# Kernel tuning notes

Hardware: AMD Instinct MI355X
Metric: run time of the kernel (lower is better)

## Reference

```python
import jax, jax.numpy as jnp
import numpy as np

N = 262144   # nodes
E = 4194304  # edges (avg degree 16)
G = 1024     # graphs in batch
F_IN, F_GCN, F_DENSE = 3, 16, 16
NEG_SLOPE = 0.01  # nn.LeakyReLU default


def _leaky(x):
    return jax.nn.leaky_relu(x, NEG_SLOPE)


def _gcn_conv(x, W, b, src, dst, ew):
    """PyG GCNConv: h = x @ W; symmetric deg-norm with self-loops (weight 1);
    out[i] = sum_{(j->i)} norm_e * h[j] + (1/deg_i) * h[i] + b."""
    h = x @ W                                   # [N, out]
    deg = jax.ops.segment_sum(ew, dst, num_segments=N) + 1.0  # +1 from self-loop
    dinv = jnp.where(deg > 0, jax.lax.rsqrt(deg), 0.0)        # deg^{-1/2}
    norm = dinv[src] * ew * dinv[dst]           # [E]
    agg = jax.ops.segment_sum(h[src] * norm[:, None], dst, num_segments=N)
    agg = agg + h * (dinv * dinv)[:, None]      # self-loop message, norm = 1/deg
    return agg + b


def setup_inputs() -> dict:
    key = jax.random.key(0)
    ks = jax.random.split(key, 24)
    inp = {
        "X": jax.random.normal(ks[0], (N, F_IN), dtype=jnp.float32),
        "Edge_index": jax.random.randint(ks[1], (2, E), 0, N, dtype=jnp.int64) if jax.config.jax_enable_x64 else jax.random.randint(ks[1], (2, E), 0, N, dtype=jnp.int32),
        "Edge_weight": jax.random.uniform(ks[2], (E,), dtype=jnp.float32),
        "Batching": jnp.sort(jax.random.randint(ks[3], (N,), 0, G, dtype=jnp.int32)),
        "num_graphs": G,
    }
    def lin(k, fi, fo):
        kw, kb = jax.random.split(k)
        s = 1.0 / np.sqrt(fi)
        return (jax.random.uniform(kw, (fi, fo), minval=-s, maxval=s, dtype=jnp.float32),
                jax.random.uniform(kb, (fo,), minval=-s, maxval=s, dtype=jnp.float32))
    inp["W1"], inp["b1"] = lin(ks[4], F_IN, F_GCN)
    inp["W2"], inp["b2"] = lin(ks[5], F_GCN, F_GCN)
    inp["Wp1"], inp["bp1"] = lin(ks[6], F_GCN, F_DENSE)
    inp["Wp2"], inp["bp2"] = lin(ks[7], F_DENSE, F_DENSE)
    inp["Wp3"], inp["bp3"] = lin(ks[8], F_DENSE, 2)
    inp["Wt1"], inp["bt1"] = lin(ks[9], F_GCN, F_DENSE)
    inp["Wt2"], inp["bt2"] = lin(ks[10], F_DENSE, F_DENSE)
    inp["Wt3"], inp["bt3"] = lin(ks[11], F_DENSE, 2)
    return inp


def reference(X, Edge_index, Edge_weight, Batching, num_graphs,
              W1, b1, W2, b2,
              Wp1, bp1, Wp2, bp2, Wp3, bp3,
              Wt1, bt1, Wt2, bt2, Wt3, bt3):
    src, dst = Edge_index[0], Edge_index[1]
    out = _leaky(_gcn_conv(X, W1, b1, src, dst, Edge_weight))
    out = _leaky(_gcn_conv(out, W2, b2, src, dst, Edge_weight))
    # global mean pool over graphs
    sums = jax.ops.segment_sum(out, Batching, num_segments=num_graphs)
    cnt = jax.ops.segment_sum(jnp.ones((out.shape[0],), out.dtype), Batching,
                              num_segments=num_graphs)
    pooled = sums / jnp.maximum(cnt, 1.0)[:, None]   # [G, 16]
    Phi = _leaky(pooled @ Wp1 + bp1)
    Phi = _leaky(Phi @ Wp2 + bp2)
    Phi = Phi @ Wp3 + bp3
    Theta = _leaky(pooled @ Wt1 + bt1)
    Theta = _leaky(Theta @ Wt2 + bt2)
    Theta = Theta @ Wt3 + bt3
    return jnp.concatenate((Phi, Theta), axis=1)   # [G, 4]
```

## Files before the change

### kernel.cpp

```cpp
#include <hip/hip_runtime.h>


#define NBUCK 512
#define BCAP  10240
#define CHUNK 4096
#define NTILE 8
#define TSH   15
#define RCAP  20

__device__ __forceinline__ float leaky(float x) { return x > 0.f ? x : 0.01f * x; }

__global__ __launch_bounds__(256) void
binA_kernel(const int* __restrict__ src, const int* __restrict__ dst,
            const float* __restrict__ ew, int* __restrict__ bucketCursor,
            int2* __restrict__ coarse, int E) {
    __shared__ int lhist[NBUCK], lbase[NBUCK], lcur[NBUCK], gbase[NBUCK];
    __shared__ int tmp[256];
    __shared__ int2 stag[CHUNK];
    __shared__ unsigned short sbuck[CHUNK];
    int t = threadIdx.x;
    int base = blockIdx.x * CHUNK;
    for (int b = t; b < NBUCK; b += 256) { lhist[b] = 0; lcur[b] = 0; }
    __syncthreads();
    int n = min(CHUNK, E - base);
    int myDst[16], mySrc[16]; float myEw[16];
#pragma unroll
    for (int k = 0; k < 16; ++k) {
        int j = t + k * 256;
        if (j < n) {
            int d = dst[base + j];
            myDst[k] = d; mySrc[k] = src[base + j]; myEw[k] = ew[base + j];
            atomicAdd(&lhist[d >> 9], 1);
        } else myDst[k] = -1;
    }
    __syncthreads();
    tmp[t] = lhist[2 * t] + lhist[2 * t + 1];
    __syncthreads();
    for (int off = 1; off < 256; off <<= 1) {
        int v = (t >= off) ? tmp[t - off] : 0;
        __syncthreads();
        tmp[t] += v;
        __syncthreads();
    }
    int pb = (t == 0) ? 0 : tmp[t - 1];
    lbase[2 * t] = pb;
    lbase[2 * t + 1] = pb + lhist[2 * t];
    __syncthreads();
    for (int b = t; b < NBUCK; b += 256) {
        int c = lhist[b];
        gbase[b] = c ? atomicAdd(&bucketCursor[b], c) : 0;
    }
    for (int k = 0; k < 16; ++k) {
        int d = myDst[k];
        if (d >= 0) {
            int b = d >> 9;
            int p = lbase[b] + atomicAdd(&lcur[b], 1);
            stag[p] = make_int2(mySrc[k] | ((d & 511) << 18), __float_as_int(myEw[k]));
            sbuck[p] = (unsigned short)b;
        }
    }
    __syncthreads();
    for (int j = t; j < n; j += 256) {
        int b = sbuck[j];
        coarse[(size_t)b * BCAP + gbase[b] + (j - lbase[b])] = stag[j];
    }
}

__global__ void bscan_kernel(const int* __restrict__ bucketCursor,
                             int* __restrict__ bucketBase, int* __restrict__ row,
                             int N, int E) {
    __shared__ int s[NBUCK];
    int t = threadIdx.x;
    int v = bucketCursor[t];
    s[t] = v;
    __syncthreads();
    for (int off = 1; off < NBUCK; off <<= 1) {
        int x = (t >= off) ? s[t - off] : 0;
        __syncthreads();
        s[t] += x;
        __syncthreads();
    }
    bucketBase[t] = s[t] - v;
    if (t == 0) row[N] = E;
}

__global__ __launch_bounds__(512, 2) void
binB_kernel(const int* __restrict__ bucketCursor, const int* __restrict__ bucketBase,
            const int2* __restrict__ coarse, int2* __restrict__ edata,
            int* __restrict__ row, float* __restrict__ dinv,
            uint4* __restrict__ tcnt) {
    __shared__ int2 sedata[BCAP];
    __shared__ int loff[NBUCK * NTILE];
    __shared__ int tmp[512];
    int b = blockIdx.x, t = threadIdx.x;
    for (int i = t; i < NBUCK * NTILE; i += 512) loff[i] = 0;
    __syncthreads();
    int cnt = bucketCursor[b];
    int gb  = bucketBase[b];
    const int2* cb = coarse + (size_t)b * BCAP;
    int2 myE[RCAP]; int myKey[RCAP];
#pragma unroll
    for (int k = 0; k < RCAP; ++k) {
        int j = t + k * 512;
        if (j < cnt) {
            int2 e = cb[j];
            myE[k] = e;
            myKey[k] = (((e.x >> 18) & 511) << 3) | ((e.x & 0x3FFFF) >> TSH);
            atomicAdd(&loff[myKey[k]], 1);
        } else myKey[k] = -1;
    }
    __syncthreads();
    int base8 = t * 8, s = 0;
#pragma unroll
    for (int k = 0; k < 8; ++k) s += loff[base8 + k];
    tmp[t] = s;
    __syncthreads();
    for (int off = 1; off < 512; off <<= 1) {
        int v = (t >= off) ? tmp[t - off] : 0;
        __syncthreads();
        tmp[t] += v;
        __syncthreads();
    }
    int run = tmp[t] - s;
    int o[9];
#pragma unroll
    for (int k = 0; k < 8; ++k) { int v = loff[base8 + k]; o[k] = run; loff[base8 + k] = run; run += v; }
    o[8] = run;
    __syncthreads();
    int node = b * 512 + t;
    row[node] = gb + o[0];
    uint4 p;
    p.x = (unsigned)(o[1] - o[0]) | ((unsigned)(o[2] - o[1]) << 16);
    p.y = (unsigned)(o[3] - o[2]) | ((unsigned)(o[4] - o[3]) << 16);
    p.z = (unsigned)(o[5] - o[4]) | ((unsigned)(o[6] - o[5]) << 16);
    p.w = (unsigned)(o[7] - o[6]) | ((unsigned)(o[8] - o[7]) << 16);
    tcnt[node] = p;
#pragma unroll
    for (int k = 0; k < RCAP; ++k) {
        if (myKey[k] >= 0) {
            int pos = atomicAdd(&loff[myKey[k]], 1);
            sedata[pos] = make_int2(myE[k].x & 0x3FFFF, myE[k].y);
        }
    }
    __syncthreads();
    for (int j = t; j < cnt; j += 512) edata[gb + j] = sedata[j];
    float dsum = 0.f;
    for (int j = o[0]; j < o[8]; ++j) dsum += __int_as_float(sedata[j].y);
    dinv[node] = rsqrtf(1.0f + dsum);
}

__global__ void node1_kernel(const float* __restrict__ X, const float* __restrict__ W1,
                             const float* __restrict__ dinv, float* __restrict__ h, int N) {
    __shared__ float w[48];
    if (threadIdx.x < 48) w[threadIdx.x] = W1[threadIdx.x];
    __syncthreads();
    int i = blockIdx.x * blockDim.x + threadIdx.x;
    if (i >= N) return;
    float x0 = X[3 * i], x1 = X[3 * i + 1], x2 = X[3 * i + 2];
    float di = dinv[i];
    float4* hp = (float4*)(h + (size_t)i * 16);
#pragma unroll
    for (int k = 0; k < 4; ++k) {
        float4 v;
        v.x = (x0 * w[4 * k + 0] + x1 * w[16 + 4 * k + 0] + x2 * w[32 + 4 * k + 0]) * di;
        v.y = (x0 * w[4 * k + 1] + x1 * w[16 + 4 * k + 1] + x2 * w[32 + 4 * k + 1]) * di;
        v.z = (x0 * w[4 * k + 2] + x1 * w[16 + 4 * k + 2] + x2 * w[32 + 4 * k + 2]) * di;
        v.w = (x0 * w[4 * k + 3] + x1 * w[16 + 4 * k + 3] + x2 * w[32 + 4 * k + 3]) * di;
        hp[k] = v;
    }
}

__global__ __launch_bounds__(512) void
aggA_kernel(const int* __restrict__ row, const uint4* __restrict__ tcnt,
            const int2* __restrict__ edata, const float* __restrict__ dinv,
            const float* __restrict__ hprime, const float* __restrict__ b1,
            const float* __restrict__ W2, float* __restrict__ h2) {
    __shared__ float w[256];
    __shared__ float bb[16];
    __shared__ float sx[128][17];
    int t = threadIdx.x;
    if (t < 256) w[t] = W2[t];
    else if (t < 272) bb[t - 256] = b1[t - 256];
    int ln = t >> 2, l = t & 3;
    int iA = blockIdx.x * 256 + ln, iB = iA + 128;
    const float4* hp = (const float4*)hprime;
    int eA = row[iA], eB = row[iB];
    uint4 cAv = tcnt[iA], cBv = tcnt[iB];
    unsigned ca[4] = {cAv.x, cAv.y, cAv.z, cAv.w};
    unsigned cb[4] = {cBv.x, cBv.y, cBv.z, cBv.w};
    float diA = dinv[iA], diB = dinv[iB];
    float4 accA = hp[(size_t)iA * 4 + l];
    float4 accB = hp[(size_t)iB * 4 + l];
#pragma unroll
    for (int tt = 0; tt < NTILE; ++tt) {
        int nA = (ca[tt >> 1] >> ((tt & 1) * 16)) & 0xFFFF;
        int nB = (cb[tt >> 1] >> ((tt & 1) * 16)) & 0xFFFF;
        for (int e = eA + nA; eA < e; ++eA) {
            int2 ed = edata[eA];
            float ewv = __int_as_float(ed.y);
            float4 v = hp[(size_t)ed.x * 4 + l];
            accA.x += v.x * ewv; accA.y += v.y * ewv;
            accA.z += v.z * ewv; accA.w += v.w * ewv;
        }
        for (int e = eB + nB; eB < e; ++eB) {
            int2 ed = edata[eB];
            float ewv = __int_as_float(ed.y);
            float4 v = hp[(size_t)ed.x * 4 + l];
            accB.x += v.x * ewv; accB.y += v.y * ewv;
            accB.z += v.z * ewv; accB.w += v.w * ewv;
        }
        __syncthreads();
    }
    sx[ln][4 * l + 0] = leaky(diA * accA.x + bb[4 * l + 0]);
    sx[ln][4 * l + 1] = leaky(diA * accA.y + bb[4 * l + 1]);
    sx[ln][4 * l + 2] = leaky(diA * accA.z + bb[4 * l + 2]);
    sx[ln][4 * l + 3] = leaky(diA * accA.w + bb[4 * l + 3]);
    __syncthreads();
    {
        float a0 = 0.f, a1 = 0.f, a2 = 0.f, a3 = 0.f;
#pragma unroll
        for (int q = 0; q < 16; ++q) {
            float xv = sx[ln][q];
            a0 += xv * w[q * 16 + 4 * l + 0];
            a1 += xv * w[q * 16 + 4 * l + 1];
            a2 += xv * w[q * 16 + 4 * l + 2];
            a3 += xv * w[q * 16 + 4 * l + 3];
        }
        ((float4*)h2)[(size_t)iA * 4 + l] = make_float4(a0 * diA, a1 * diA, a2 * diA, a3 * diA);
    }
    __syncthreads();
    sx[ln][4 * l + 0] = leaky(diB * accB.x + bb[4 * l + 0]);
    sx[ln][4 * l + 1] = leaky(diB * accB.y + bb[4 * l + 1]);
    sx[ln][4 * l + 2] = leaky(diB * accB.z + bb[4 * l + 2]);
    sx[ln][4 * l + 3] = leaky(diB * accB.w + bb[4 * l + 3]);
    __syncthreads();
    {
        float a0 = 0.f, a1 = 0.f, a2 = 0.f, a3 = 0.f;
#pragma unroll
        for (int q = 0; q < 16; ++q) {
            float xv = sx[ln][q];
            a0 += xv * w[q * 16 + 4 * l + 0];
            a1 += xv * w[q * 16 + 4 * l + 1];
            a2 += xv * w[q * 16 + 4 * l + 2];
            a3 += xv * w[q * 16 + 4 * l + 3];
        }
        ((float4*)h2)[(size_t)iB * 4 + l] = make_float4(a0 * diB, a1 * diB, a2 * diB, a3 * diB);
    }
}

__global__ __launch_bounds__(512) void
aggB_kernel(const int* __restrict__ row, const uint4* __restrict__ tcnt,
            const int2* __restrict__ edata, const float* __restrict__ dinv,
            const float* __restrict__ h2prime, float* __restrict__ agg2) {
    int t = threadIdx.x;
    int ln = t >> 2, l = t & 3;
    int iA = blockIdx.x * 256 + ln, iB = iA + 128;
    const float4* hp = (const float4*)h2prime;
    int eA = row[iA], eB = row[iB];
    uint4 cAv = tcnt[iA], cBv = tcnt[iB];
    unsigned ca[4] = {cAv.x, cAv.y, cAv.z, cAv.w};
    unsigned cb[4] = {cBv.x, cBv.y, cBv.z, cBv.w};
    float diA = dinv[iA], diB = dinv[iB];
    float4 accA = hp[(size_t)iA * 4 + l];
    float4 accB = hp[(size_t)iB * 4 + l];
#pragma unroll
    for (int tt = 0; tt < NTILE; ++tt) {
        int nA = (ca[tt >> 1] >> ((tt & 1) * 16)) & 0xFFFF;
        int nB = (cb[tt >> 1] >> ((tt & 1) * 16)) & 0xFFFF;
        for (int e = eA + nA; eA < e; ++eA) {
            int2 ed = edata[eA];
            float ewv = __int_as_float(ed.y);
            float4 v = hp[(size_t)ed.x * 4 + l];
            accA.x += v.x * ewv; accA.y += v.y * ewv;
            accA.z += v.z * ewv; accA.w += v.w * ewv;
        }
        for (int e = eB + nB; eB < e; ++eB) {
            int2 ed = edata[eB];
            float ewv = __int_as_float(ed.y);
            float4 v = hp[(size_t)ed.x * 4 + l];
            accB.x += v.x * ewv; accB.y += v.y * ewv;
            accB.z += v.z * ewv; accB.w += v.w * ewv;
        }
        __syncthreads();
    }
    ((float4*)agg2)[(size_t)iA * 4 + l] =
        make_float4(accA.x * diA, accA.y * diA, accA.z * diA, accA.w * diA);
    ((float4*)agg2)[(size_t)iB * 4 + l] =
        make_float4(accB.x * diB, accB.y * diB, accB.z * diB, accB.w * diB);
}

__device__ void head_mlp(const float* pooled,
                         const float* __restrict__ Wa, const float* __restrict__ ba,
                         const float* __restrict__ Wb, const float* __restrict__ bb,
                         const float* __restrict__ Wc, const float* __restrict__ bc,
                         float* o) {
    float t[16], u[16];
#pragma unroll
    for (int f = 0; f < 16; ++f) {
        float a = ba[f];
        for (int k = 0; k < 16; ++k) a += pooled[k] * Wa[k * 16 + f];
        t[f] = leaky(a);
    }
#pragma unroll
    for (int f = 0; f < 16; ++f) {
        float a = bb[f];
        for (int k = 0; k < 16; ++k) a += t[k] * Wb[k * 16 + f];
        u[f] = leaky(a);
    }
    float o0 = bc[0], o1 = bc[1];
    for (int k = 0; k < 16; ++k) { o0 += u[k] * Wc[2 * k]; o1 += u[k] * Wc[2 * k + 1]; }
    o[0] = o0; o[1] = o1;
}

__global__ void pool_head_kernel(const float* __restrict__ agg2, const float* __restrict__ b2,
                                 const int* __restrict__ batching, int N,
                                 const float* __restrict__ Wp1, const float* __restrict__ bp1,
                                 const float* __restrict__ Wp2, const float* __restrict__ bp2,
                                 const float* __restrict__ Wp3, const float* __restrict__ bp3,
                                 const float* __restrict__ Wt1, const float* __restrict__ bt1,
                                 const float* __restrict__ Wt2, const float* __restrict__ bt2,
                                 const float* __restrict__ Wt3, const float* __restrict__ bt3,
                                 float* __restrict__ out) {
    int g = blockIdx.x;
    __shared__ int bounds[2];
    if (threadIdx.x < 2) {
        int v = g + (int)threadIdx.x;
        int lo = 0, hi = N;
        while (lo < hi) { int m = (lo + hi) >> 1; if (batching[m] < v) lo = m + 1; else hi = m; }
        bounds[threadIdx.x] = lo;
    }
    __syncthreads();
    int lo = bounds[0], hi = bounds[1];
    int f = threadIdx.x & 15, r = threadIdx.x >> 4;
    float bf = b2[f];
    float acc = 0.f;
    for (int i = lo + r; i < hi; i += 16) acc += leaky(agg2[(size_t)i * 16 + f] + bf);
    __shared__ float red[16][17];
    red[r][f] = acc;
    __syncthreads();
    __shared__ float pooled[16];
    if (r == 0) {
        float s = 0.f;
#pragma unroll
        for (int k = 0; k < 16; ++k) s += red[k][f];
        pooled[f] = s / fmaxf((float)(hi - lo), 1.0f);
    }
    __syncthreads();
    if (threadIdx.x == 0) {
        float o[2];
        head_mlp(pooled, Wp1, bp1, Wp2, bp2, Wp3, bp3, o);
        out[4 * g + 0] = o[0]; out[4 * g + 1] = o[1];
    } else if (threadIdx.x == 1) {
        float o[2];
        head_mlp(pooled, Wt1, bt1, Wt2, bt2, Wt3, bt3, o);
        out[4 * g + 2] = o[0]; out[4 * g + 3] = o[1];
    }
}

extern "C" void kernel_launch(void* const* d_in, const int* in_sizes, int n_in,
                              void* d_out, int out_size, void* d_ws, size_t ws_size,
                              hipStream_t stream) {
    const float* X        = (const float*)d_in[0];
    const int*   ei       = (const int*)d_in[1];
    const float* ew       = (const float*)d_in[2];
    const int*   batching = (const int*)d_in[3];
    const float* W1  = (const float*)d_in[5];  const float* b1  = (const float*)d_in[6];
    const float* W2  = (const float*)d_in[7];  const float* b2  = (const float*)d_in[8];
    const float* Wp1 = (const float*)d_in[9];  const float* bp1 = (const float*)d_in[10];
    const float* Wp2 = (const float*)d_in[11]; const float* bp2 = (const float*)d_in[12];
    const float* Wp3 = (const float*)d_in[13]; const float* bp3 = (const float*)d_in[14];
    const float* Wt1 = (const float*)d_in[15]; const float* bt1 = (const float*)d_in[16];
    const float* Wt2 = (const float*)d_in[17]; const float* bt2 = (const float*)d_in[18];
    const float* Wt3 = (const float*)d_in[19]; const float* bt3 = (const float*)d_in[20];

    const int N = in_sizes[3];
    const int E = in_sizes[2];
    const int G = out_size / 4;
    const int* src = ei;
    const int* dst = ei + E;

    char* ws = (char*)d_ws;
    size_t off = 0;
    int2*  edata = (int2*)(ws + off);  off += (size_t)E * 8;
    char*  regionA = ws + off;         off += (size_t)N * 64 * 3;
    int2*  coarse = (int2*)regionA;
    float* hprime = (float*)regionA;
    float* h2     = (float*)(regionA + (size_t)N * 64);
    float* agg2   = (float*)(regionA + (size_t)N * 128);
    int*   bucketCursor = (int*)(ws + off); off += NBUCK * 4;
    int*   bucketBase   = (int*)(ws + off); off += NBUCK * 4;
    int*   row   = (int*)(ws + off);   off += (size_t)(N + 4) * 4;
    float* dinv  = (float*)(ws + off); off += (size_t)N * 4;
    uint4* tcnt  = (uint4*)(ws + off); off += (size_t)N * 16;
    float* out   = (float*)d_out;

    hipMemsetAsync(bucketCursor, 0, NBUCK * 4, stream);

    const int tb = 256;
    binA_kernel<<<(E + CHUNK - 1) / CHUNK, tb, 0, stream>>>(src, dst, ew, bucketCursor, coarse, E);
    bscan_kernel<<<1, NBUCK, 0, stream>>>(bucketCursor, bucketBase, row, N, E);
    binB_kernel<<<NBUCK, 512, 0, stream>>>(bucketCursor, bucketBase, coarse, edata, row, dinv, tcnt);
    node1_kernel<<<(N + tb - 1) / tb, tb, 0, stream>>>(X, W1, dinv, hprime, N);
    aggA_kernel<<<N / 256, 512, 0, stream>>>(row, tcnt, edata, dinv, hprime, b1, W2, h2);
    aggB_kernel<<<N / 256, 512, 0, stream>>>(row, tcnt, edata, dinv, h2, agg2);
    pool_head_kernel<<<G, tb, 0, stream>>>(agg2, b2, batching, N,
                                           Wp1, bp1, Wp2, bp2, Wp3, bp3,
                                           Wt1, bt1, Wt2, bt2, Wt3, bt3, out);
}
```

Before: 374.9 us.

## Aggregate raw 3-feature inputs in layer 1 and apply W1 on the fly

Instead of precomputing h' = X·W1·dinv as 16 floats per node, a pack kernel stores (x0,x1,x2,dinv) as one float4 per node. The first aggregation gathers that 16-byte record per edge and applies W1 in registers. This cuts gather bytes per edge and removes the 64-byte-per-node h' buffer. The tiled loop with its per-tile __syncthreads is replaced by a plain interleaved while loop over the row range. The trade-off is more FMAs per edge, and each of the 4 lanes per node redundantly gathers the same float4.

```diff
diff --git a/kernel.cpp b/kernel.cpp
--- a/kernel.cpp
+++ b/kernel.cpp
@@ -149,72 +149,70 @@
     dinv[node] = rsqrtf(1.0f + dsum);
 }
 
-__global__ void node1_kernel(const float* __restrict__ X, const float* __restrict__ W1,
-                             const float* __restrict__ dinv, float* __restrict__ h, int N) {
-    __shared__ float w[48];
-    if (threadIdx.x < 48) w[threadIdx.x] = W1[threadIdx.x];
-    __syncthreads();
+__global__ void pack_kernel(const float* __restrict__ X, const float* __restrict__ dinv,
+                            float4* __restrict__ Xp, int N) {
     int i = blockIdx.x * blockDim.x + threadIdx.x;
     if (i >= N) return;
-    float x0 = X[3 * i], x1 = X[3 * i + 1], x2 = X[3 * i + 2];
-    float di = dinv[i];
-    float4* hp = (float4*)(h + (size_t)i * 16);
-#pragma unroll
-    for (int k = 0; k < 4; ++k) {
-        float4 v;
-        v.x = (x0 * w[4 * k + 0] + x1 * w[16 + 4 * k + 0] + x2 * w[32 + 4 * k + 0]) * di;
-        v.y = (x0 * w[4 * k + 1] + x1 * w[16 + 4 * k + 1] + x2 * w[32 + 4 * k + 1]) * di;
-        v.z = (x0 * w[4 * k + 2] + x1 * w[16 + 4 * k + 2] + x2 * w[32 + 4 * k + 2]) * di;
-        v.w = (x0 * w[4 * k + 3] + x1 * w[16 + 4 * k + 3] + x2 * w[32 + 4 * k + 3]) * di;
-        hp[k] = v;
-    }
+    Xp[i] = make_float4(X[3 * i], X[3 * i + 1], X[3 * i + 2], dinv[i]);
 }
 
 __global__ __launch_bounds__(512) void
-aggA_kernel(const int* __restrict__ row, const uint4* __restrict__ tcnt,
-            const int2* __restrict__ edata, const float* __restrict__ dinv,
-            const float* __restrict__ hprime, const float* __restrict__ b1,
-            const float* __restrict__ W2, float* __restrict__ h2) {
+aggA_kernel(const int* __restrict__ row, const int2* __restrict__ edata,
+            const float4* __restrict__ Xp, const float* __restrict__ W1,
+            const float* __restrict__ b1, const float* __restrict__ W2,
+            float* __restrict__ h2) {
+    __shared__ float w1s[48];
     __shared__ float w[256];
     __shared__ float bb[16];
     __shared__ float sx[128][17];
     int t = threadIdx.x;
     if (t < 256) w[t] = W2[t];
     else if (t < 272) bb[t - 256] = b1[t - 256];
+    else if (t >= 288 && t < 336) w1s[t - 288] = W1[t - 288];
+    __syncthreads();
     int ln = t >> 2, l = t & 3;
+    float w1r0[4], w1r1[4], w1r2[4];
+#pragma unroll
+    for (int c = 0; c < 4; ++c) {
+        w1r0[c] = w1s[0 * 16 + 4 * l + c];
+        w1r1[c] = w1s[1 * 16 + 4 * l + c];
+        w1r2[c] = w1s[2 * 16 + 4 * l + c];
+    }
     int iA = blockIdx.x * 256 + ln, iB = iA + 128;
-    const float4* hp = (const float4*)hprime;
-    int eA = row[iA], eB = row[iB];
-    uint4 cAv = tcnt[iA], cBv = tcnt[iB];
-    unsigned ca[4] = {cAv.x, cAv.y, cAv.z, cAv.w};
-    unsigned cb[4] = {cBv.x, cBv.y, cBv.z, cBv.w};
-    float diA = dinv[iA], diB = dinv[iB];
-    float4 accA = hp[(size_t)iA * 4 + l];
-    float4 accB = hp[(size_t)iB * 4 + l];
-#pragma unroll
-    for (int tt = 0; tt < NTILE; ++tt) {
-        int nA = (ca[tt >> 1] >> ((tt & 1) * 16)) & 0xFFFF;
-        int nB = (cb[tt >> 1] >> ((tt & 1) * 16)) & 0xFFFF;
-        for (int e = eA + nA; eA < e; ++eA) {
-            int2 ed = edata[eA];
-            float ewv = __int_as_float(ed.y);
-            float4 v = hp[(size_t)ed.x * 4 + l];
-            accA.x += v.x * ewv; accA.y += v.y * ewv;
-            accA.z += v.z * ewv; accA.w += v.w * ewv;
-        }
-        for (int e = eB + nB; eB < e; ++eB) {
-            int2 ed = edata[eB];
-            float ewv = __int_as_float(ed.y);
-            float4 v = hp[(size_t)ed.x * 4 + l];
-            accB.x += v.x * ewv; accB.y += v.y * ewv;
-            accB.z += v.z * ewv; accB.w += v.w * ewv;
-        }
-        __syncthreads();
-    }
-    sx[ln][4 * l + 0] = leaky(diA * accA.x + bb[4 * l + 0]);
-    sx[ln][4 * l + 1] = leaky(diA * accA.y + bb[4 * l + 1]);
-    sx[ln][4 * l + 2] = leaky(diA * accA.z + bb[4 * l + 2]);
-    sx[ln][4 * l + 3] = leaky(diA * accA.w + bb[4 * l + 3]);
+    int eA = row[iA], eAend = row[iA + 1];
+    int eB = row[iB], eBend = row[iB + 1];
+    float4 xpA = Xp[iA], xpB = Xp[iB];
+    float diA = xpA.w, diB = xpB.w;
+    float accA[4], accB[4];
+#pragma unroll
+    for (int c = 0; c < 4; ++c) {
+        accA[c] = (xpA.x * w1r0[c] + xpA.y * w1r1[c] + xpA.z * w1r2[c]) * diA;
+        accB[c] = (xpB.x * w1r0[c] + xpB.y * w1r1[c] + xpB.z * w1r2[c]) * diB;
+    }
+    while (eA < eAend || eB < eBend) {
+        if (eA < eAend) {
+            int2 ed = edata[eA++];
+            float4 xs = Xp[ed.x];
+            float f = __int_as_float(ed.y) * xs.w;
+            float f0 = xs.x * f, f1 = xs.y * f, f2 = xs.z * f;
+#pragma unroll
+            for (int c = 0; c < 4; ++c)
+                accA[c] += f0 * w1r0[c] + f1 * w1r1[c] + f2 * w1r2[c];
+        }
+        if (eB < eBend) {
+            int2 ed = edata[eB++];
+            float4 xs = Xp[ed.x];
+            float f = __int_as_float(ed.y) * xs.w;
+            float f0 = xs.x * f, f1 = xs.y * f, f2 = xs.z * f;
+#pragma unroll
+            for (int c = 0; c < 4; ++c)
+                accB[c] += f0 * w1r0[c] + f1 * w1r1[c] + f2 * w1r2[c];
+        }
+    }
+    sx[ln][4 * l + 0] = leaky(diA * accA[0] + bb[4 * l + 0]);
+    sx[ln][4 * l + 1] = leaky(diA * accA[1] + bb[4 * l + 1]);
+    sx[ln][4 * l + 2] = leaky(diA * accA[2] + bb[4 * l + 2]);
+    sx[ln][4 * l + 3] = leaky(diA * accA[3] + bb[4 * l + 3]);
     __syncthreads();
     {
         float a0 = 0.f, a1 = 0.f, a2 = 0.f, a3 = 0.f;
@@ -229,10 +227,10 @@
         ((float4*)h2)[(size_t)iA * 4 + l] = make_float4(a0 * diA, a1 * diA, a2 * diA, a3 * diA);
     }
     __syncthreads();
-    sx[ln][4 * l + 0] = leaky(diB * accB.x + bb[4 * l + 0]);
-    sx[ln][4 * l + 1] = leaky(diB * accB.y + bb[4 * l + 1]);
-    sx[ln][4 * l + 2] = leaky(diB * accB.z + bb[4 * l + 2]);
-    sx[ln][4 * l + 3] = leaky(diB * accB.w + bb[4 * l + 3]);
+    sx[ln][4 * l + 0] = leaky(diB * accB[0] + bb[4 * l + 0]);
+    sx[ln][4 * l + 1] = leaky(diB * accB[1] + bb[4 * l + 1]);
+    sx[ln][4 * l + 2] = leaky(diB * accB[2] + bb[4 * l + 2]);
+    sx[ln][4 * l + 3] = leaky(diB * accB[3] + bb[4 * l + 3]);
     __syncthreads();
     {
         float a0 = 0.f, a1 = 0.f, a2 = 0.f, a3 = 0.f;
@@ -384,9 +382,9 @@
     int2*  edata = (int2*)(ws + off);  off += (size_t)E * 8;
     char*  regionA = ws + off;         off += (size_t)N * 64 * 3;
     int2*  coarse = (int2*)regionA;
-    float* hprime = (float*)regionA;
-    float* h2     = (float*)(regionA + (size_t)N * 64);
-    float* agg2   = (float*)(regionA + (size_t)N * 128);
+    float* h2     = (float*)regionA;
+    float* agg2   = (float*)(regionA + (size_t)N * 64);
+    float4* Xp    = (float4*)(regionA + (size_t)N * 128);
     int*   bucketCursor = (int*)(ws + off); off += NBUCK * 4;
     int*   bucketBase   = (int*)(ws + off); off += NBUCK * 4;
     int*   row   = (int*)(ws + off);   off += (size_t)(N + 4) * 4;
@@ -400,8 +398,8 @@
     binA_kernel<<<(E + CHUNK - 1) / CHUNK, tb, 0, stream>>>(src, dst, ew, bucketCursor, coarse, E);
     bscan_kernel<<<1, NBUCK, 0, stream>>>(bucketCursor, bucketBase, row, N, E);
     binB_kernel<<<NBUCK, 512, 0, stream>>>(bucketCursor, bucketBase, coarse, edata, row, dinv, tcnt);
-    node1_kernel<<<(N + tb - 1) / tb, tb, 0, stream>>>(X, W1, dinv, hprime, N);
-    aggA_kernel<<<N / 256, 512, 0, stream>>>(row, tcnt, edata, dinv, hprime, b1, W2, h2);
+    pack_kernel<<<(N + tb - 1) / tb, tb, 0, stream>>>(X, dinv, Xp, N);
+    aggA_kernel<<<N / 256, 512, 0, stream>>>(row, edata, Xp, W1, b1, W2, h2);
     aggB_kernel<<<N / 256, 512, 0, stream>>>(row, tcnt, edata, dinv, h2, agg2);
     pool_head_kernel<<<G, tb, 0, stream>>>(agg2, b2, batching, N,
                                            Wp1, bp1, Wp2, bp2, Wp3, bp3,
```

Result: slower. 382.4 us (+2.0%).
